# Kernel tuning notes

Hardware: AMD Instinct MI355X
Metric: run time of the kernel (lower is better)

The kernel has to match this reference:

```python
import jax, jax.numpy as jnp
import numpy as np

HIDDEN = 512
EXP = 2048  # hidden * expansion_factor(4)

def _glorot(key, shape):
    fan_in = shape[0]
    return jax.random.normal(key, shape, dtype=jnp.float32) / np.sqrt(fan_in)

def setup_inputs() -> dict:
    key = jax.random.key(0)
    ks = jax.random.split(key, 6)
    B, S = 4, 4096
    return {
        "x": jax.random.normal(ks[0], (B, S, HIDDEN), dtype=jnp.float32),
        "W_in1": _glorot(ks[1], (HIDDEN, EXP)),
        "b_in1": jnp.zeros((EXP,), jnp.float32),
        "W_in2": _glorot(ks[2], (HIDDEN, EXP)),
        "b_in2": jnp.zeros((EXP,), jnp.float32),
        "W_z": _glorot(ks[3], (EXP, EXP)),
        "b_z": jnp.zeros((EXP,), jnp.float32),
        "W_h": _glorot(ks[4], (EXP, EXP)),
        "b_h": jnp.zeros((EXP,), jnp.float32),
        "W_out": _glorot(ks[5], (EXP, HIDDEN)),
        "b_out": jnp.zeros((HIDDEN,), jnp.float32),
    }

def _min_gru(x_in, W_z, b_z, W_h, b_h):
    # minGRU: h_t = (1 - z_t) * h_{t-1} + z_t * h_tilde_t, h_0 = 0
    z = jax.nn.sigmoid(jnp.einsum("bse,ef->bsf", x_in, W_z) + b_z)
    h_tilde = jnp.einsum("bse,ef->bsf", x_in, W_h) + b_h
    a = 1.0 - z          # decay coeff
    b = z * h_tilde      # input term
    def combine(c1, c2):
        a1, b1 = c1
        a2, b2 = c2
        return (a1 * a2, b1 * a2 + b2)
    _, h = jax.lax.associative_scan(combine, (a, b), axis=1)
    return h

def reference(x, W_in1, b_in1, W_in2, b_in2, W_z, b_z, W_h, b_h, W_out, b_out):
    x_in = jax.nn.silu(jnp.einsum("bsd,de->bse", x, W_in1) + b_in1)
    x_skip = jax.nn.silu(jnp.einsum("bsd,de->bse", x, W_in2) + b_in2)
    h = _min_gru(x_in, W_z, b_z, W_h, b_h)
    return jnp.einsum("bse,ed->bsd", x_skip + h, W_out) + b_out
```

## Files before the change

kernel.cpp:

```cpp
#include <hip/hip_runtime.h>
#include <hip/hip_bf16.h>


typedef __bf16 bf16x8 __attribute__((ext_vector_type(8)));
typedef __bf16 bf16x4 __attribute__((ext_vector_type(4)));
typedef float  f32x4  __attribute__((ext_vector_type(4)));

#define DEVINL __device__ __forceinline__

DEVINL void async_ld16(const __bf16* g, __bf16* l) {
    __builtin_amdgcn_global_load_lds(
        (const __attribute__((address_space(1))) void*)g,
        (__attribute__((address_space(3))) void*)l, 16, 0, 0);
}

DEVINL float fsigmoid(float v) { return 1.0f / (1.0f + __expf(-v)); }

template <int MODE>
__global__ __launch_bounds__(512, 4)
void gemm4(const __bf16* __restrict__ A, const __bf16* __restrict__ Bt,
           const float* __restrict__ bias, const float* __restrict__ bias2,
           void* __restrict__ out, void* __restrict__ out2, int N, int K,
           int bps, int seg_stride, int row_off)
{
    struct KL { __bf16 A[128 * 32]; __bf16 B[256 * 32]; };
    __shared__ union SM4 {
        KL kl[2];
        __bf16 ct[64 * 264];
    } sm;
    const int tid = threadIdx.x;
    const int bx = blockIdx.x;
    const int seg = bx / bps;
    const int within = bx - seg * bps;
    const int gm0 = row_off + seg * seg_stride + within * 128;
    const int om0 = bx * 128;
    const int n0 = blockIdx.y * 256;

    const int rA = tid >> 2,         kA = (tid & 3) ^ ((tid >> 3) & 3);
    const int c0 = tid, c1 = tid + 512;
    const int rB0 = c0 >> 2,         kB0 = (c0 & 3) ^ ((c0 >> 3) & 3);
    const int rB1 = c1 >> 2,         kB1 = (c1 & 3) ^ ((c1 >> 3) & 3);
    const __bf16* Ag  = A  + (size_t)(gm0 + rA)  * K + kA  * 8;
    const __bf16* Bg0 = Bt + (size_t)(n0 + rB0) * K + kB0 * 8;
    const __bf16* Bg1 = Bt + (size_t)(n0 + rB1) * K + kB1 * 8;

    const int lane = tid & 63;
    const int wave = tid >> 6;
    const int wm = wave >> 2;
    const int wn = wave & 3;
    const int quad = lane >> 4;
    const int r = lane & 15;
    const int swz = (quad ^ ((r >> 1) & 3)) * 8;

    f32x4 acc[4][4] = {};

    const int T = K >> 5;

    auto stage = [&](int t, int b) {
        const int kt = t << 5;
        async_ld16(Ag  + kt, sm.kl[b].A + tid * 8);
        async_ld16(Bg0 + kt, sm.kl[b].B + c0 * 8);
        async_ld16(Bg1 + kt, sm.kl[b].B + c1 * 8);
    };

    stage(0, 0);

    for (int t = 0; t < T; ++t) {
        const int cur = t & 1;
        if (t + 1 < T) {
            stage(t + 1, cur ^ 1);
            asm volatile("s_waitcnt vmcnt(3)\n\ts_barrier" ::: "memory");
        } else {
            asm volatile("s_waitcnt vmcnt(0)\n\ts_barrier" ::: "memory");
        }

        const __bf16* ap = sm.kl[cur].A + (wm * 64 + r) * 32 + swz;
        const __bf16* bp = sm.kl[cur].B + (wn * 64 + r) * 32 + swz;
        bf16x8 af[4], bf_[4];
#pragma unroll
        for (int m = 0; m < 4; ++m) af[m] = *(const bf16x8*)(ap + m * 512);
#pragma unroll
        for (int n = 0; n < 4; ++n) bf_[n] = *(const bf16x8*)(bp + n * 512);

        __builtin_amdgcn_s_setprio(1);
#pragma unroll
        for (int m = 0; m < 4; ++m)
#pragma unroll
            for (int n = 0; n < 4; ++n)
                acc[m][n] = __builtin_amdgcn_mfma_f32_16x16x32_bf16(
                    af[m], bf_[n], acc[m][n], 0, 0, 0);
        __builtin_amdgcn_s_setprio(0);

        asm volatile("s_waitcnt lgkmcnt(0)\n\ts_barrier" ::: "memory");
    }

    const bool lo = n0 < 2048;
    __bf16* dst;
    int cb;
    size_t stride;
    if (MODE == 0) {
        dst = lo ? (__bf16*)out : (__bf16*)out2;
        cb = lo ? n0 : n0 - 2048;
        stride = 2048;
    } else {
        dst = (__bf16*)out;
        cb = n0;
        stride = (size_t)N;
    }
    float bvj[4];
#pragma unroll
    for (int nf = 0; nf < 4; ++nf) {
        const int gc = n0 + wn * 64 + nf * 16 + r;
        bvj[nf] = lo ? bias[gc] : bias2[gc - 2048];
    }

#pragma unroll
    for (int p = 0; p < 2; ++p) {
        if (wm == p) {
#pragma unroll
            for (int mm = 0; mm < 4; ++mm)
#pragma unroll
                for (int nf = 0; nf < 4; ++nf)
#pragma unroll
                    for (int k = 0; k < 4; ++k) {
                        const float v = acc[mm][nf][k] + bvj[nf];
                        const __bf16 o = (MODE == 0) ? (__bf16)(v * fsigmoid(v))
                                                     : (__bf16)v;
                        sm.ct[(mm * 16 + quad * 4 + k) * 264 +
                              (wn * 64 + nf * 16 + r)] = o;
                    }
        }
        __syncthreads();
#pragma unroll
        for (int q = 0; q < 4; ++q) {
            const int chunk = q * 512 + tid;
            const int trow = chunk >> 5;
            const int tc = (chunk & 31) * 8;
            const bf16x8 vv = *(const bf16x8*)(sm.ct + trow * 264 + tc);
            *(bf16x8*)(dst + (size_t)(om0 + p * 64 + trow) * stride + cb + tc) = vv;
        }
        __syncthreads();
    }
}

template <int MODE>
__global__ __launch_bounds__(512, 2)
void gemm3k(const __bf16* __restrict__ A, const __bf16* __restrict__ Bt,
            const float* __restrict__ bias, const float* __restrict__ bias2,
            void* __restrict__ out, void* __restrict__ out2, int N, int K,
            int bps, int seg_stride, int row_off)
{
    struct KL { __bf16 A[256 * 64]; __bf16 B[256 * 64]; };
    __shared__ union SM3K {
        KL kl[2];
        __bf16 ct[64 * 264];
    } sm;
    const int tid = threadIdx.x;
    const int bx = blockIdx.x;
    const int seg = bx / bps;
    const int within = bx - seg * bps;
    const int gm0 = row_off + seg * seg_stride + within * 256;
    const int om0 = bx * 256;
    const int n0 = blockIdx.y * 256;

    int rA[4], kA[4];
#pragma unroll
    for (int j = 0; j < 4; ++j) {
        const int s = tid + 512 * j;
        rA[j] = s >> 3;
        kA[j] = (s & 7) ^ (rA[j] & 7);
    }
    const __bf16* Agp[4];
    const __bf16* Bgp[4];
#pragma unroll
    for (int j = 0; j < 4; ++j) {
        Agp[j] = A  + (size_t)(gm0 + rA[j]) * K + kA[j] * 8;
        Bgp[j] = Bt + (size_t)(n0 + rA[j]) * K + kA[j] * 8;
    }

    const int lane = tid & 63;
    const int wave = tid >> 6;
    const int wm = wave >> 2;
    const int wn = wave & 3;
    const int quad = lane >> 4;
    const int r = lane & 15;

    f32x4 acc[8][4] = {};

    const int T = K >> 6;

    auto stage = [&](int t, int b) {
        const int kt = t << 6;
#pragma unroll
        for (int j = 0; j < 4; ++j)
            async_ld16(Agp[j] + kt, sm.kl[b].A + (tid + 512 * j) * 8);
#pragma unroll
        for (int j = 0; j < 4; ++j)
            async_ld16(Bgp[j] + kt, sm.kl[b].B + (tid + 512 * j) * 8);
    };

    stage(0, 0);

    const int swz0 = ((0 * 4 + quad) ^ (r & 7)) * 8;
    const int swz1 = ((1 * 4 + quad) ^ (r & 7)) * 8;

    for (int t = 0; t < T; ++t) {
        const int cur = t & 1;
        if (t + 1 < T) {
            stage(t + 1, cur ^ 1);
            asm volatile("s_waitcnt vmcnt(8)\n\ts_barrier" ::: "memory");
        } else {
            asm volatile("s_waitcnt vmcnt(0)\n\ts_barrier" ::: "memory");
        }

        const __bf16* apb = sm.kl[cur].A + (wm * 128 + r) * 64;
        const __bf16* bpb = sm.kl[cur].B + (wn * 64 + r) * 64;

#pragma unroll
        for (int ks = 0; ks < 2; ++ks) {
            const int swz = ks ? swz1 : swz0;
            bf16x8 af[8], bf_[4];
#pragma unroll
            for (int m = 0; m < 8; ++m)
                af[m] = *(const bf16x8*)(apb + m * 1024 + swz);
#pragma unroll
            for (int n = 0; n < 4; ++n)
                bf_[n] = *(const bf16x8*)(bpb + n * 1024 + swz);

            __builtin_amdgcn_s_setprio(1);
#pragma unroll
            for (int m = 0; m < 8; ++m)
#pragma unroll
                for (int n = 0; n < 4; ++n)
                    acc[m][n] = __builtin_amdgcn_mfma_f32_16x16x32_bf16(
                        af[m], bf_[n], acc[m][n], 0, 0, 0);
            __builtin_amdgcn_s_setprio(0);
        }

        asm volatile("s_waitcnt lgkmcnt(0)\n\ts_barrier" ::: "memory");
    }

    __syncthreads();

    const bool lo = n0 < 2048;
    __bf16* dst = (__bf16*)out;
    const int cb = n0;
    const size_t stride = (size_t)N;
    float bvj[4];
#pragma unroll
    for (int nf = 0; nf < 4; ++nf) {
        const int gc = n0 + wn * 64 + nf * 16 + r;
        bvj[nf] = lo ? bias[gc] : bias2[gc - 2048];
    }

#pragma unroll
    for (int p = 0; p < 4; ++p) {
        if (wm == (p >> 1)) {
            const int mb = (p & 1) * 4;
#pragma unroll
            for (int mm = 0; mm < 4; ++mm)
#pragma unroll
                for (int nf = 0; nf < 4; ++nf)
#pragma unroll
                    for (int k = 0; k < 4; ++k) {
                        const float v = acc[mb + mm][nf][k] + bvj[nf];
                        sm.ct[(mm * 16 + quad * 4 + k) * 264 +
                              (wn * 64 + nf * 16 + r)] = (__bf16)v;
                    }
        }
        __syncthreads();
#pragma unroll
        for (int q = 0; q < 4; ++q) {
            const int chunk = q * 512 + tid;
            const int trow = chunk >> 5;
            const int tc = (chunk & 31) * 8;
            const bf16x8 vv = *(const bf16x8*)(sm.ct + trow * 264 + tc);
            *(bf16x8*)(dst + (size_t)(om0 + p * 64 + trow) * stride + cb + tc) = vv;
        }
        __syncthreads();
    }
}

template <int MODE>
__global__ __launch_bounds__(256)
void gemm_bt64(const __bf16* __restrict__ A, const __bf16* __restrict__ Bt,
               const float* __restrict__ bias, const float* __restrict__ bias2,
               void* __restrict__ out, void* __restrict__ out2, int N, int K,
               int bps, int seg_stride, int row_off)
{
    struct KL64 { __bf16 A[128 * 64]; __bf16 B[128 * 64]; };
    __shared__ union SMB64 {
        KL64 kl[2];
        float  ctf[32 * 132];
    } sm;
    const int tid = threadIdx.x;
    const int bx = blockIdx.x;
    const int seg = bx / bps;
    const int within = bx - seg * bps;
    const int gm0 = row_off + seg * seg_stride + within * 128;
    const int om0 = bx * 128;
    const int n0 = blockIdx.y * 128;

    int rS[4], kS[4];
#pragma unroll
    for (int j = 0; j < 4; ++j) {
        const int s = tid + 256 * j;
        rS[j] = s >> 3;
        kS[j] = (s & 7) ^ (rS[j] & 7);
    }
    const __bf16* Agp[4];
    const __bf16* Bgp[4];
#pragma unroll
    for (int j = 0; j < 4; ++j) {
        Agp[j] = A  + (size_t)(gm0 + rS[j]) * K + kS[j] * 8;
        Bgp[j] = Bt + (size_t)(n0 + rS[j]) * K + kS[j] * 8;
    }

    const int lane = tid & 63;
    const int wave = tid >> 6;
    const int wrow = (wave >> 1) * 64;
    const int wcol = (wave & 1) * 64;
    const int quad = lane >> 4;
    const int r = lane & 15;

    f32x4 acc[4][4] = {};

    const int T = K >> 6;

    auto stage = [&](int t, int b) {
        const int kt = t << 6;
#pragma unroll
        for (int j = 0; j < 4; ++j)
            async_ld16(Agp[j] + kt, sm.kl[b].A + (tid + 256 * j) * 8);
#pragma unroll
        for (int j = 0; j < 4; ++j)
            async_ld16(Bgp[j] + kt, sm.kl[b].B + (tid + 256 * j) * 8);
    };

    stage(0, 0);

    const int swz0 = ((0 * 4 + quad) ^ (r & 7)) * 8;
    const int swz1 = ((1 * 4 + quad) ^ (r & 7)) * 8;

    for (int t = 0; t < T; ++t) {
        const int cur = t & 1;
        if (t + 1 < T) {
            stage(t + 1, cur ^ 1);
            asm volatile("s_waitcnt vmcnt(8)\n\ts_barrier" ::: "memory");
        } else {
            asm volatile("s_waitcnt vmcnt(0)\n\ts_barrier" ::: "memory");
        }

        const __bf16* apb = sm.kl[cur].A + (wrow + r) * 64;
        const __bf16* bpb = sm.kl[cur].B + (wcol + r) * 64;

#pragma unroll
        for (int ks = 0; ks < 2; ++ks) {
            const int swz = ks ? swz1 : swz0;
            bf16x8 af[4], bf_[4];
#pragma unroll
            for (int m = 0; m < 4; ++m)
                af[m] = *(const bf16x8*)(apb + m * 1024 + swz);
#pragma unroll
            for (int n = 0; n < 4; ++n)
                bf_[n] = *(const bf16x8*)(bpb + n * 1024 + swz);

            __builtin_amdgcn_s_setprio(1);
#pragma unroll
            for (int m = 0; m < 4; ++m)
#pragma unroll
                for (int n = 0; n < 4; ++n)
                    acc[m][n] = __builtin_amdgcn_mfma_f32_16x16x32_bf16(
                        af[m], bf_[n], acc[m][n], 0, 0, 0);
            __builtin_amdgcn_s_setprio(0);
        }

        asm volatile("s_waitcnt lgkmcnt(0)\n\ts_barrier" ::: "memory");
    }

    {
        float bvj[4];
#pragma unroll
        for (int j = 0; j < 4; ++j)
            bvj[j] = bias[n0 + wcol + j * 16 + r];
#pragma unroll
        for (int p = 0; p < 4; ++p) {
#pragma unroll
            for (int j = 0; j < 4; ++j)
#pragma unroll
                for (int k = 0; k < 4; ++k)
                    sm.ctf[((wave >> 1) * 16 + quad * 4 + k) * 132 +
                           (wcol + j * 16 + r)] = acc[p][j][k] + bvj[j];
            __syncthreads();
#pragma unroll
            for (int q = 0; q < 4; ++q) {
                const int chunk = q * 256 + tid;
                const int trow = chunk >> 5;
                const int tc4 = (chunk & 31) * 4;
                const f32x4 vv = *(const f32x4*)(sm.ctf + trow * 132 + tc4);
                const int grow = om0 + (trow >> 4) * 64 + p * 16 + (trow & 15);
                *(f32x4*)((float*)out + (size_t)grow * N + n0 + tc4) = vv;
            }
            __syncthreads();
        }
    }
}

#define SSEG 32
#define SCOLS 32
__global__ __launch_bounds__(1024)
void scan_kernel(const __bf16* __restrict__ raw, __bf16* __restrict__ xskip,
                 float* __restrict__ carry, int CS, int S, int t0, int first)
{
    __shared__ float Als[SSEG][SCOLS];
    __shared__ float Bls[SSEG][SCOLS];
    const int lane = threadIdx.x & (SCOLS - 1);
    const int w = threadIdx.x >> 5;
    const int nb8 = gridDim.x >> 3;
    const int lin = (blockIdx.x & 7) * nb8 + (blockIdx.x >> 3);
    const int gpb = 2048 / SCOLS;
    const int batch = lin / gpb;
    const int col = (lin - batch * gpb) * SCOLS + lane;
    const int L = CS / SSEG;
    const int tbeg = w * L;

    const size_t rbase = ((size_t)batch * CS + tbeg) * 4096 + col;

    float av[32], bv[32];
    float A = 1.0f, Bv = 0.0f;
    {
        size_t idx = rbase;
#pragma unroll
        for (int t = 0; t < 32; ++t, idx += 4096) {
            const float z = fsigmoid((float)raw[idx]);
            const float b = z * (float)raw[idx + 2048];
            const float a = 1.0f - z;
            av[t] = a;
            bv[t] = b;
            Bv = a * Bv + b;
            A *= a;
        }
    }
    Als[w][lane] = A;
    Bls[w][lane] = Bv;
    __syncthreads();

    const int ch = batch * 2048 + col;
    float h = first ? 0.0f : carry[ch];
    for (int s = 0; s < w; ++s)
        h = Als[s][lane] * h + Bls[s][lane];
    if (w == SSEG - 1)
        carry[ch] = A * h + Bv;

    {
        size_t gidx = ((size_t)batch * S + t0 + tbeg) * 2048 + col;
#pragma unroll
        for (int t = 0; t < 32; ++t, gidx += 2048) {
            h = av[t] * h + bv[t];
            xskip[gidx] = (__bf16)((float)xskip[gidx] + h);
        }
    }
}

__global__ __launch_bounds__(256)
void prep_kernel(const float* __restrict__ x, __bf16* __restrict__ xb,
                 const float* __restrict__ W_in1, const float* __restrict__ W_in2,
                 __bf16* __restrict__ Wt12,
                 const float* __restrict__ W_z, const float* __restrict__ W_h,
                 __bf16* __restrict__ Wtzh,
                 const float* __restrict__ W_out, __bf16* __restrict__ Wto)
{
    __shared__ float tile[32][33];
    int bid = blockIdx.x;
    if (bid < 8192) {
        const int i = bid * 256 + threadIdx.x;
        const float4 v = ((const float4*)x)[i];
        bf16x4 o;
        o[0] = (__bf16)v.x; o[1] = (__bf16)v.y;
        o[2] = (__bf16)v.z; o[3] = (__bf16)v.w;
        ((bf16x4*)xb)[i] = o;
        return;
    }
    bid -= 8192;
    const float* W;
    __bf16* dst;
    int K, N, nb, kb;
    if (bid < 2048) {
        const int z = bid >> 10, rem = bid & 1023;
        W = z ? W_in2 : W_in1;
        dst = Wt12 + (size_t)z * 512 * 2048;
        K = 512; N = 2048;
        nb = (rem & 63) * 32; kb = (rem >> 6) * 32;
    } else if (bid < 2048 + 8192) {
        const int b2 = bid - 2048;
        const int z = b2 >> 12, rem = b2 & 4095;
        W = z ? W_h : W_z;
        dst = Wtzh + (size_t)z * 2048 * 2048;
        K = 2048; N = 2048;
        nb = (rem & 63) * 32; kb = (rem >> 6) * 32;
    } else {
        const int b3 = bid - (2048 + 8192);
        W = W_out; dst = Wto;
        K = 2048; N = 512;
        nb = (b3 & 15) * 32; kb = (b3 >> 4) * 32;
    }
    const int tx = threadIdx.x & 31;
    const int ty = threadIdx.x >> 5;
#pragma unroll
    for (int i = 0; i < 32; i += 8)
        tile[ty + i][tx] = W[(size_t)(kb + ty + i) * N + nb + tx];
    __syncthreads();
#pragma unroll
    for (int i = 0; i < 32; i += 8)
        dst[(size_t)(nb + ty + i) * K + kb + tx] = (__bf16)tile[tx][ty + i];
}

extern "C" void kernel_launch(void* const* d_in, const int* in_sizes, int n_in,
                              void* d_out, int out_size, void* d_ws, size_t ws_size,
                              hipStream_t stream)
{
    const float* x     = (const float*)d_in[0];
    const float* W_in1 = (const float*)d_in[1];
    const float* b_in1 = (const float*)d_in[2];
    const float* W_in2 = (const float*)d_in[3];
    const float* b_in2 = (const float*)d_in[4];
    const float* W_z   = (const float*)d_in[5];
    const float* b_z   = (const float*)d_in[6];
    const float* W_h   = (const float*)d_in[7];
    const float* b_h   = (const float*)d_in[8];
    const float* W_out = (const float*)d_in[9];
    const float* b_out = (const float*)d_in[10];

    const int B = 4, S = 4096, H = 512, E = 2048;
    const int M = B * S;
    const int CS = 1024;
    const int NC = S / CS;
    const int MC = B * CS;

    const size_t MiB = 1024 * 1024;
    const size_t NEEDED = 183 * MiB;
    if (ws_size < NEEDED) return;

    char* ws = (char*)d_ws;
    __bf16* xb    = (__bf16*)(ws + 0);
    __bf16* rawzh = (__bf16*)(ws + 0);
    float*  carry = (float*) (ws + 32 * MiB);
    __bf16* xin   = (__bf16*)(ws + 33 * MiB);
    __bf16* xskip = (__bf16*)(ws + 97 * MiB);
    __bf16* Wt12  = (__bf16*)(ws + 161 * MiB);
    __bf16* Wtzh  = (__bf16*)(ws + 165 * MiB);
    __bf16* Wto   = (__bf16*)(ws + 181 * MiB);

    prep_kernel<<<8192 + 2048 + 8192 + 1024, 256, 0, stream>>>(
        x, xb, W_in1, W_in2, Wt12, W_z, W_h, Wtzh, W_out, Wto);

    gemm4<0><<<dim3(M / 128, 2 * E / 256), 512, 0, stream>>>(
        xb, Wt12, b_in1, b_in2, xin, xskip, 2 * E, H, M / 128, 0, 0);

    for (int c = 0; c < NC; ++c) {
        const int row_off = c * CS;
        gemm3k<4><<<dim3(MC / 256, 2 * E / 256), 512, 0, stream>>>(
            xin, Wtzh, b_z, b_h, rawzh, nullptr, 2 * E, E, CS / 256, S, row_off);
        scan_kernel<<<(B * E) / SCOLS, 1024, 0, stream>>>(
            rawzh, xskip, carry, CS, S, row_off, c == 0);
    }

    gemm_bt64<3><<<dim3(M / 128, H / 128), 256, 0, stream>>>(
        xskip, Wto, b_out, nullptr, (float*)d_out, nullptr, H, E, M / 128, 0, 0);
}
```

Before: 574.7 us.

## Interleave staged global-to-LDS prefetch with per-phase MFMA blocks in GEMM main loop

The K-loop now splits the next tile's async global-to-LDS copy into four chunks of two loads each. Each chunk is issued inside one of four compute phases, and each phase handles two M-fragments against the B fragments loaded once at the start of the tile. The goal is to spread memory issue across the MFMA work and to hold fewer A fragments in registers at once. The cost is more workgroup barriers per tile (about eight instead of two) and finer-grained LDS waits, which may add sync stalls with 512-thread blocks.

```diff
diff --git a/kernel.cpp b/kernel.cpp
--- a/kernel.cpp
+++ b/kernel.cpp
@@ -189,55 +189,87 @@
 
     const int T = K >> 6;
 
-    auto stage = [&](int t, int b) {
+    auto stagelet = [&](int t, int b, int p) {
         const int kt = t << 6;
-#pragma unroll
-        for (int j = 0; j < 4; ++j)
-            async_ld16(Agp[j] + kt, sm.kl[b].A + (tid + 512 * j) * 8);
-#pragma unroll
-        for (int j = 0; j < 4; ++j)
-            async_ld16(Bgp[j] + kt, sm.kl[b].B + (tid + 512 * j) * 8);
+        if (p == 0) {
+            async_ld16(Agp[0] + kt, sm.kl[b].A + (tid      ) * 8);
+            async_ld16(Agp[1] + kt, sm.kl[b].A + (tid + 512) * 8);
+        } else if (p == 1) {
+            async_ld16(Agp[2] + kt, sm.kl[b].A + (tid + 1024) * 8);
+            async_ld16(Agp[3] + kt, sm.kl[b].A + (tid + 1536) * 8);
+        } else if (p == 2) {
+            async_ld16(Bgp[0] + kt, sm.kl[b].B + (tid      ) * 8);
+            async_ld16(Bgp[1] + kt, sm.kl[b].B + (tid + 512) * 8);
+        } else {
+            async_ld16(Bgp[2] + kt, sm.kl[b].B + (tid + 1024) * 8);
+            async_ld16(Bgp[3] + kt, sm.kl[b].B + (tid + 1536) * 8);
+        }
     };
 
-    stage(0, 0);
+#pragma unroll
+    for (int p = 0; p < 4; ++p) stagelet(0, 0, p);
 
     const int swz0 = ((0 * 4 + quad) ^ (r & 7)) * 8;
     const int swz1 = ((1 * 4 + quad) ^ (r & 7)) * 8;
 
     for (int t = 0; t < T; ++t) {
         const int cur = t & 1;
-        if (t + 1 < T) {
-            stage(t + 1, cur ^ 1);
-            asm volatile("s_waitcnt vmcnt(8)\n\ts_barrier" ::: "memory");
-        } else {
-            asm volatile("s_waitcnt vmcnt(0)\n\ts_barrier" ::: "memory");
-        }
-
+        const bool pre = (t + 1) < T;
         const __bf16* apb = sm.kl[cur].A + (wm * 128 + r) * 64;
         const __bf16* bpb = sm.kl[cur].B + (wn * 64 + r) * 64;
 
-#pragma unroll
-        for (int ks = 0; ks < 2; ++ks) {
-            const int swz = ks ? swz1 : swz0;
-            bf16x8 af[8], bf_[4];
-#pragma unroll
-            for (int m = 0; m < 8; ++m)
-                af[m] = *(const bf16x8*)(apb + m * 1024 + swz);
-#pragma unroll
-            for (int n = 0; n < 4; ++n)
-                bf_[n] = *(const bf16x8*)(bpb + n * 1024 + swz);
-
+        bf16x8 bfr[2][4];
+
+        if (pre) {
+            stagelet(t + 1, cur ^ 1, 0);
+            asm volatile("s_waitcnt vmcnt(2)" ::: "memory");
+        } else {
+            asm volatile("s_waitcnt vmcnt(0)" ::: "memory");
+        }
+        __builtin_amdgcn_s_barrier();
+        {
+            bf16x8 a00 = *(const bf16x8*)(apb + 0 * 1024 + swz0);
+            bf16x8 a01 = *(const bf16x8*)(apb + 0 * 1024 + swz1);
+            bf16x8 a10 = *(const bf16x8*)(apb + 1 * 1024 + swz0);
+            bf16x8 a11 = *(const bf16x8*)(apb + 1 * 1024 + swz1);
+#pragma unroll
+            for (int n = 0; n < 4; ++n) {
+                bfr[0][n] = *(const bf16x8*)(bpb + n * 1024 + swz0);
+                bfr[1][n] = *(const bf16x8*)(bpb + n * 1024 + swz1);
+            }
+            asm volatile("s_waitcnt lgkmcnt(0)" ::: "memory");
             __builtin_amdgcn_s_setprio(1);
 #pragma unroll
-            for (int m = 0; m < 8; ++m)
-#pragma unroll
-                for (int n = 0; n < 4; ++n)
-                    acc[m][n] = __builtin_amdgcn_mfma_f32_16x16x32_bf16(
-                        af[m], bf_[n], acc[m][n], 0, 0, 0);
+            for (int n = 0; n < 4; ++n) {
+                acc[0][n] = __builtin_amdgcn_mfma_f32_16x16x32_bf16(a00, bfr[0][n], acc[0][n], 0, 0, 0);
+                acc[0][n] = __builtin_amdgcn_mfma_f32_16x16x32_bf16(a01, bfr[1][n], acc[0][n], 0, 0, 0);
+                acc[1][n] = __builtin_amdgcn_mfma_f32_16x16x32_bf16(a10, bfr[0][n], acc[1][n], 0, 0, 0);
+                acc[1][n] = __builtin_amdgcn_mfma_f32_16x16x32_bf16(a11, bfr[1][n], acc[1][n], 0, 0, 0);
+            }
             __builtin_amdgcn_s_setprio(0);
         }
-
-        asm volatile("s_waitcnt lgkmcnt(0)\n\ts_barrier" ::: "memory");
+        __builtin_amdgcn_s_barrier();
+
+#pragma unroll
+        for (int p = 1; p < 4; ++p) {
+            bf16x8 a00 = *(const bf16x8*)(apb + (2 * p    ) * 1024 + swz0);
+            bf16x8 a01 = *(const bf16x8*)(apb + (2 * p    ) * 1024 + swz1);
+            bf16x8 a10 = *(const bf16x8*)(apb + (2 * p + 1) * 1024 + swz0);
+            bf16x8 a11 = *(const bf16x8*)(apb + (2 * p + 1) * 1024 + swz1);
+            if (pre) stagelet(t + 1, cur ^ 1, p);
+            __builtin_amdgcn_s_barrier();
+            asm volatile("s_waitcnt lgkmcnt(0)" ::: "memory");
+            __builtin_amdgcn_s_setprio(1);
+#pragma unroll
+            for (int n = 0; n < 4; ++n) {
+                acc[2 * p][n]     = __builtin_amdgcn_mfma_f32_16x16x32_bf16(a00, bfr[0][n], acc[2 * p][n], 0, 0, 0);
+                acc[2 * p][n]     = __builtin_amdgcn_mfma_f32_16x16x32_bf16(a01, bfr[1][n], acc[2 * p][n], 0, 0, 0);
+                acc[2 * p + 1][n] = __builtin_amdgcn_mfma_f32_16x16x32_bf16(a10, bfr[0][n], acc[2 * p + 1][n], 0, 0, 0);
+                acc[2 * p + 1][n] = __builtin_amdgcn_mfma_f32_16x16x32_bf16(a11, bfr[1][n], acc[2 * p + 1][n], 0, 0, 0);
+            }
+            __builtin_amdgcn_s_setprio(0);
+            __builtin_amdgcn_s_barrier();
+        }
     }
 
     __syncthreads();
```

New measurement: 566.6 us (median of 2 runs). Within noise of the previous version (-1.4%).
